# Kernel tuning notes

Measured on AMD Instinct MI355X. Metric: run time of the kernel, lower is better.

The kernel has to match this reference:

```python
import jax, jax.numpy as jnp
import numpy as np

N = 50000        # n_nodes
E = 800000       # n_edges (avg degree 16)
H = 64           # hidden_size
ALPHA = 0.5      # CRF alpha
BETA = 0.5       # CRF beta
N_LAYER = 2      # args.crf_layer
GAMMA = 0.2      # LeakyReLU negative slope


def setup_inputs() -> dict:
    key = jax.random.key(0)
    k = jax.random.split(key, 5)
    emb = jax.random.normal(k[0], (N, H), jnp.float32)
    W_fc = jax.random.normal(k[1], (H, H), jnp.float32) / np.sqrt(H)
    attn_fc_w = jax.random.normal(k[2], (1, 2 * H), jnp.float32) / np.sqrt(2 * H)
    src = jax.random.randint(k[3], (E,), 0, N, dtype=jnp.int32)
    dst = jax.random.randint(k[4], (E,), 0, N, dtype=jnp.int32)
    return {"emb": emb, "W_fc": W_fc, "attn_fc_w": attn_fc_w, "src": src, "dst": dst}


def _segment_softmax(e, dst, n):
    # softmax over incoming edges of each destination node (DGL mailbox softmax)
    m = jax.ops.segment_max(e, dst, num_segments=n)
    m = jnp.where(jnp.isfinite(m), m, 0.0)  # nodes with no in-edges
    ex = jnp.exp(e - m[dst])
    denom = jax.ops.segment_sum(ex, dst, num_segments=n)
    return ex / jnp.maximum(denom[dst], 1e-16)


def reference(emb, W_fc, attn_fc_w, src, dst):
    # attn_fc(concat(z_src, z_dst)) split into two per-node projections
    a_src = attn_fc_w[0, :H]
    a_dst = attn_fc_w[0, H:]
    h = emb
    e = None
    for _ in range(N_LAYER):
        z = h @ W_fc.T                              # [N, H] emb_attn
        e = (z @ a_src)[src] + (z @ a_dst)[dst]     # [E] edge logits
        e = jnp.where(e > 0, e, GAMMA * e)          # LeakyReLU(gamma)
        att = _segment_softmax(e, dst, N)           # [E]
        crf = jax.ops.segment_sum(att[:, None] * h[src], dst, num_segments=N)  # [N, H]
        h = (ALPHA * emb + BETA * crf) / (ALPHA + BETA)
    # training loss (is_train=True); reuses last layer's edge logits e
    loss_a = jnp.sum((h - emb) ** 2, axis=-1)                     # [N]
    att = _segment_softmax(e, dst, N)
    diff = jnp.sqrt(jnp.sum((h[dst] - h[src]) ** 2, axis=-1) + 1e-12)  # [E] L2 norm
    loss_b = jax.ops.segment_sum(att * diff, dst, num_segments=N)  # [N]
    loss = jnp.mean(ALPHA * loss_a + BETA * loss_b)
    return h, loss
```

## Files before the change

### kernel.cpp

```cpp
#include <hip/hip_runtime.h>

#define NNODES 50000
#define NEDGES 800000
#define HDIM 64
#define CAP 64
#define GAMMA 0.2f
#define SCAN_B 256
#define SCAN_NB ((NNODES + SCAN_B - 1) / SCAN_B)
#define LOSS_GRID 2048
#define NPART 8
#define NODES_PER_PART ((NNODES + NPART - 1) / NPART)
#define FILL_SLICES 192
#define E4 (NEDGES / 4)
#define CHUNK ((E4 + FILL_SLICES - 1) / FILL_SLICES)

typedef unsigned short u16;
typedef unsigned int u32;

__device__ __forceinline__ u16 f2bf(float f) {
    u32 u = __float_as_uint(f);
    u32 r = (u + 0x7FFFu + ((u >> 16) & 1u)) >> 16;
    return (u16)r;
}
__device__ __forceinline__ float bflo(u32 u) { return __uint_as_float(u << 16); }
__device__ __forceinline__ float bfhi(u32 u) { return __uint_as_float(u & 0xFFFF0000u); }

__device__ __forceinline__ float wave_sum(float v) {
    #pragma unroll
    for (int off = 32; off; off >>= 1) v += __shfl_xor(v, off, 64);
    return v;
}
__device__ __forceinline__ float wave_max(float v) {
    #pragma unroll
    for (int off = 32; off; off >>= 1) v = fmaxf(v, __shfl_xor(v, off, 64));
    return v;
}
__device__ __forceinline__ int wave_sum_i(int v) {
    #pragma unroll
    for (int off = 32; off; off >>= 1) v += __shfl_xor(v, off, 64);
    return v;
}
__device__ __forceinline__ float group8_sum(float v) {
    v += __shfl_xor(v, 1, 64);
    v += __shfl_xor(v, 2, 64);
    v += __shfl_xor(v, 4, 64);
    return v;
}

__global__ __launch_bounds__(256) void k_init(int* __restrict__ cursor,
                                              float* __restrict__ lossAcc,
                                              const float* __restrict__ Wfc,
                                              const float* __restrict__ attn,
                                              float* __restrict__ ws, float* __restrict__ wd) {
    int t = threadIdx.x;
    int idx = blockIdx.x * 256 + t;
    if (idx < NNODES) cursor[idx] = 0;
    if (blockIdx.x == gridDim.x - 1) {
        if (t >= 80 && t < 96) lossAcc[t - 80] = 0.f;
        if (t >= 128) {
            int tt = t - 128;
            int k = tt & 63;
            const float* av = attn + ((tt >= 64) ? HDIM : 0);
            float s = 0.f;
            for (int j = 0; j < HDIM; ++j) s += Wfc[j * HDIM + k] * av[j];
            if (tt < 64) ws[k] = s; else wd[k] = s;
        }
    }
}

__global__ __launch_bounds__(256) void k_fillx(const int4* __restrict__ src4,
                                               const int4* __restrict__ dst4,
                                               int* __restrict__ cursor,
                                               u16* __restrict__ padded) {
    const int part = blockIdx.x & (NPART - 1);
    const int slice = blockIdx.x >> 3;
    const int lo = slice * CHUNK;
    const int hi = min(lo + CHUNK, E4);
    const int plo = part * NODES_PER_PART;
    const int phi = plo + NODES_PER_PART;
    for (int i = lo + threadIdx.x; i < hi; i += 256) {
        int4 d = dst4[i];
        bool mx = d.x >= plo && d.x < phi;
        bool my = d.y >= plo && d.y < phi;
        bool mz = d.z >= plo && d.z < phi;
        bool mw = d.w >= plo && d.w < phi;
        if (mx | my | mz | mw) {
            int4 s = src4[i];
            if (mx) { int p0 = atomicAdd(&cursor[d.x], 1); if (p0 < CAP) padded[d.x * CAP + p0] = (u16)s.x; }
            if (my) { int p1 = atomicAdd(&cursor[d.y], 1); if (p1 < CAP) padded[d.y * CAP + p1] = (u16)s.y; }
            if (mz) { int p2 = atomicAdd(&cursor[d.z], 1); if (p2 < CAP) padded[d.z * CAP + p2] = (u16)s.z; }
            if (mw) { int p3 = atomicAdd(&cursor[d.w], 1); if (p3 < CAP) padded[d.w * CAP + p3] = (u16)s.w; }
        }
    }
}

__global__ __launch_bounds__(256) void k_scan1z(const int* __restrict__ deg,
                                                int* __restrict__ blockSums,
                                                const float* __restrict__ emb,
                                                const float* __restrict__ ws,
                                                const float* __restrict__ wd,
                                                u16* __restrict__ emb_bf,
                                                float* __restrict__ zs, float* __restrict__ zd) {
    int t = threadIdx.x;
    if (blockIdx.x < SCAN_NB) {
        int idx = blockIdx.x * SCAN_B + t;
        int v = (idx < NNODES) ? min(deg[idx], CAP) : 0;
        int wsum = wave_sum_i(v);
        __shared__ int part[4];
        if ((t & 63) == 0) part[t >> 6] = wsum;
        __syncthreads();
        if (t == 0) blockSums[blockIdx.x] = part[0] + part[1] + part[2] + part[3];
    }
    int tid = blockIdx.x * blockDim.x + threadIdx.x;
    int wid = tid >> 6;
    int lane = tid & 63;
    if (wid < NNODES) {
        float v = emb[wid * HDIM + lane];
        emb_bf[wid * HDIM + lane] = f2bf(v);
        float a = wave_sum(v * ws[lane]);
        float b = wave_sum(v * wd[lane]);
        if (lane == 0) { zs[wid] = a; zd[wid] = b; }
    }
}

__global__ __launch_bounds__(SCAN_B) void k_scan3(const int* __restrict__ deg,
                                                  const int* __restrict__ blockSums,
                                                  int* __restrict__ row_ptr) {
    __shared__ int s[SCAN_B];
    int t = threadIdx.x;
    int bv = (t < SCAN_NB) ? blockSums[t] : 0;
    s[t] = bv;
    __syncthreads();
    for (int off = 1; off < SCAN_B; off <<= 1) {
        int x = (t >= off) ? s[t - off] : 0;
        __syncthreads();
        s[t] += x;
        __syncthreads();
    }
    int blockOff = (blockIdx.x > 0) ? s[blockIdx.x - 1] : 0;
    __syncthreads();
    int idx = blockIdx.x * SCAN_B + t;
    int v = (idx < NNODES) ? min(deg[idx], CAP) : 0;
    s[t] = v;
    __syncthreads();
    for (int off = 1; off < SCAN_B; off <<= 1) {
        int x = (t >= off) ? s[t - off] : 0;
        __syncthreads();
        s[t] += x;
        __syncthreads();
    }
    if (idx < NNODES) {
        int excl = s[t] - v + blockOff;
        row_ptr[idx] = excl;
        if (idx == NNODES - 1) row_ptr[NNODES] = excl + v;
    }
}

template <bool STORE_ATT, bool COMPUTE_Z, bool WRITE_F32, bool STORE_LA, bool COMPACT>
__global__ __launch_bounds__(256) void k_layer(const u16* __restrict__ hbf_in,
                                               const float* __restrict__ emb,
                                               const int* __restrict__ deg,
                                               const int* __restrict__ row_ptr,
                                               const u16* __restrict__ padded,
                                               const float* __restrict__ zs,
                                               const float* __restrict__ zd,
                                               float* __restrict__ att_csr,
                                               u16* __restrict__ csr_c,
                                               u16* __restrict__ dmap_c,
                                               float* __restrict__ h_out,
                                               u16* __restrict__ hbf_out,
                                               const float* __restrict__ ws,
                                               const float* __restrict__ wd,
                                               float* __restrict__ zs_out,
                                               float* __restrict__ zd_out,
                                               float* __restrict__ la) {
    int wid = (blockIdx.x * blockDim.x + threadIdx.x) >> 6;
    int lane = threadIdx.x & 63;
    if (wid >= NNODES) return;
    int ne = min(deg[wid], CAP);
    int s0 = 0;
    if (STORE_ATT || COMPACT) s0 = row_ptr[wid];
    float zdn = zd[wid];
    const int sub8 = lane >> 3, q8 = lane & 7;
    float acc[8];
    #pragma unroll
    for (int i = 0; i < 8; ++i) acc[i] = 0.f;

    int s = 0; float e = -INFINITY;
    bool valid = lane < ne;
    if (valid) {
        s = padded[(size_t)wid * CAP + lane];
        float z = zs[s] + zdn;
        e = z > 0.f ? z : GAMMA * z;
    }
    float m = wave_max(e);
    float ex = valid ? __expf(e - m) : 0.f;
    float dsum = wave_sum(ex);
    float inv = 1.f / fmaxf(dsum, 1e-16f);
    if (STORE_ATT && valid) att_csr[s0 + lane] = ex * inv;
    if (COMPACT && valid) {
        csr_c[s0 + lane] = (u16)s;
        dmap_c[s0 + lane] = (u16)wid;
    }
    for (int j = 0; j < ne; j += 16) {
        int ja = j + sub8, jb = j + 8 + sub8;
        float wa = __shfl(ex, ja, 64);
        float wb = __shfl(ex, jb, 64);
        int ta = __shfl(s, ja, 64);
        int tb = __shfl(s, jb, 64);
        const uint4 ra = *(const uint4*)&hbf_in[(size_t)ta * HDIM + 8 * q8];
        const uint4 rb = *(const uint4*)&hbf_in[(size_t)tb * HDIM + 8 * q8];
        acc[0] += wa * bflo(ra.x) + wb * bflo(rb.x);
        acc[1] += wa * bfhi(ra.x) + wb * bfhi(rb.x);
        acc[2] += wa * bflo(ra.y) + wb * bflo(rb.y);
        acc[3] += wa * bfhi(ra.y) + wb * bfhi(rb.y);
        acc[4] += wa * bflo(ra.z) + wb * bflo(rb.z);
        acc[5] += wa * bfhi(ra.z) + wb * bfhi(rb.z);
        acc[6] += wa * bflo(ra.w) + wb * bflo(rb.w);
        acc[7] += wa * bfhi(ra.w) + wb * bfhi(rb.w);
    }
    #pragma unroll
    for (int off = 8; off <= 32; off <<= 1) {
        #pragma unroll
        for (int i = 0; i < 8; ++i) acc[i] += __shfl_xor(acc[i], off, 64);
    }
    float hv[8];
    #pragma unroll
    for (int i = 0; i < 8; ++i) hv[i] = 0.f;
    float lap = 0.f;
    if (sub8 == 0) {
        const float4 e0 = *(const float4*)&emb[(size_t)wid * HDIM + 8 * q8];
        const float4 e1 = *(const float4*)&emb[(size_t)wid * HDIM + 8 * q8 + 4];
        hv[0] = 0.5f * (e0.x + acc[0] * inv);
        hv[1] = 0.5f * (e0.y + acc[1] * inv);
        hv[2] = 0.5f * (e0.z + acc[2] * inv);
        hv[3] = 0.5f * (e0.w + acc[3] * inv);
        hv[4] = 0.5f * (e1.x + acc[4] * inv);
        hv[5] = 0.5f * (e1.y + acc[5] * inv);
        hv[6] = 0.5f * (e1.z + acc[6] * inv);
        hv[7] = 0.5f * (e1.w + acc[7] * inv);
        if (WRITE_F32) {
            *(float4*)&h_out[(size_t)wid * HDIM + 8 * q8]     = make_float4(hv[0], hv[1], hv[2], hv[3]);
            *(float4*)&h_out[(size_t)wid * HDIM + 8 * q8 + 4] = make_float4(hv[4], hv[5], hv[6], hv[7]);
        }
        uint4 o;
        o.x = (u32)f2bf(hv[0]) | ((u32)f2bf(hv[1]) << 16);
        o.y = (u32)f2bf(hv[2]) | ((u32)f2bf(hv[3]) << 16);
        o.z = (u32)f2bf(hv[4]) | ((u32)f2bf(hv[5]) << 16);
        o.w = (u32)f2bf(hv[6]) | ((u32)f2bf(hv[7]) << 16);
        *(uint4*)&hbf_out[(size_t)wid * HDIM + 8 * q8] = o;
        if (STORE_LA) {
            float d0 = hv[0] - e0.x, d1 = hv[1] - e0.y, d2 = hv[2] - e0.z, d3 = hv[3] - e0.w;
            float d4 = hv[4] - e1.x, d5 = hv[5] - e1.y, d6 = hv[6] - e1.z, d7 = hv[7] - e1.w;
            lap = d0 * d0 + d1 * d1 + d2 * d2 + d3 * d3 +
                  d4 * d4 + d5 * d5 + d6 * d6 + d7 * d7;
        }
    }
    if (STORE_LA) {
        float lsum = wave_sum(lap);
        if (lane == 0) la[wid] = lsum;
    }
    if (COMPUTE_Z) {
        float pa = 0.f, pb = 0.f;
        if (sub8 == 0) {
            const float4 w0 = *(const float4*)&ws[8 * q8];
            const float4 w1 = *(const float4*)&ws[8 * q8 + 4];
            const float4 d0 = *(const float4*)&wd[8 * q8];
            const float4 d1 = *(const float4*)&wd[8 * q8 + 4];
            pa = hv[0] * w0.x + hv[1] * w0.y + hv[2] * w0.z + hv[3] * w0.w +
                 hv[4] * w1.x + hv[5] * w1.y + hv[6] * w1.z + hv[7] * w1.w;
            pb = hv[0] * d0.x + hv[1] * d0.y + hv[2] * d0.z + hv[3] * d0.w +
                 hv[4] * d1.x + hv[5] * d1.y + hv[6] * d1.z + hv[7] * d1.w;
        }
        float a = wave_sum(pa);
        float b = wave_sum(pb);
        if (lane == 0) { zs_out[wid] = a; zd_out[wid] = b; }
    }
}

__global__ __launch_bounds__(256) void k_loss(const float* __restrict__ la,
                                              const u16* __restrict__ hbf,
                                              const u16* __restrict__ csr_src,
                                              const u16* __restrict__ dst_map,
                                              const float* __restrict__ att_csr,
                                              float* __restrict__ acc) {
    const int lane = threadIdx.x & 63;
    const int wib = threadIdx.x >> 6;
    const int gtid = blockIdx.x * blockDim.x + threadIdx.x;
    const int nthreads = gridDim.x * blockDim.x;
    const int gw = gtid >> 6;
    const int nwaves = nthreads >> 6;
    const int sub8 = lane >> 3, q8 = lane & 7;
    float lb = 0.f;

    for (int i = gtid; i < NNODES / 4; i += nthreads) {
        const float4 v = *(const float4*)&la[i * 4];
        lb += 0.5f * (v.x + v.y + v.z + v.w);
    }
    if ((NNODES & 3) != 0 && gtid < (NNODES & 3)) lb += 0.5f * la[(NNODES & ~3) + gtid];

    for (int g = gw; g < NEDGES / 32; g += nwaves) {
        int e0 = g * 32 + sub8;
        int e1 = e0 + 8, e2 = e0 + 16, e3 = e0 + 24;
        int s0i = csr_src[e0], d0i = dst_map[e0];
        int s1i = csr_src[e1], d1i = dst_map[e1];
        int s2i = csr_src[e2], d2i = dst_map[e2];
        int s3i = csr_src[e3], d3i = dst_map[e3];
        const uint4 rs0 = *(const uint4*)&hbf[(size_t)s0i * HDIM + 8 * q8];
        const uint4 rd0 = *(const uint4*)&hbf[(size_t)d0i * HDIM + 8 * q8];
        const uint4 rs1 = *(const uint4*)&hbf[(size_t)s1i * HDIM + 8 * q8];
        const uint4 rd1 = *(const uint4*)&hbf[(size_t)d1i * HDIM + 8 * q8];
        const uint4 rs2 = *(const uint4*)&hbf[(size_t)s2i * HDIM + 8 * q8];
        const uint4 rd2 = *(const uint4*)&hbf[(size_t)d2i * HDIM + 8 * q8];
        const uint4 rs3 = *(const uint4*)&hbf[(size_t)s3i * HDIM + 8 * q8];
        const uint4 rd3 = *(const uint4*)&hbf[(size_t)d3i * HDIM + 8 * q8];
        float a0 = bflo(rd0.x) - bflo(rs0.x), a1 = bfhi(rd0.x) - bfhi(rs0.x);
        float a2 = bflo(rd0.y) - bflo(rs0.y), a3 = bfhi(rd0.y) - bfhi(rs0.y);
        float a4 = bflo(rd0.z) - bflo(rs0.z), a5 = bfhi(rd0.z) - bfhi(rs0.z);
        float a6 = bflo(rd0.w) - bflo(rs0.w), a7 = bfhi(rd0.w) - bfhi(rs0.w);
        float b0 = bflo(rd1.x) - bflo(rs1.x), b1 = bfhi(rd1.x) - bfhi(rs1.x);
        float b2 = bflo(rd1.y) - bflo(rs1.y), b3 = bfhi(rd1.y) - bfhi(rs1.y);
        float b4 = bflo(rd1.z) - bflo(rs1.z), b5 = bfhi(rd1.z) - bfhi(rs1.z);
        float b6 = bflo(rd1.w) - bflo(rs1.w), b7 = bfhi(rd1.w) - bfhi(rs1.w);
        float c0 = bflo(rd2.x) - bflo(rs2.x), c1 = bfhi(rd2.x) - bfhi(rs2.x);
        float c2 = bflo(rd2.y) - bflo(rs2.y), c3 = bfhi(rd2.y) - bfhi(rs2.y);
        float c4 = bflo(rd2.z) - bflo(rs2.z), c5 = bfhi(rd2.z) - bfhi(rs2.z);
        float c6 = bflo(rd2.w) - bflo(rs2.w), c7 = bfhi(rd2.w) - bfhi(rs2.w);
        float g0 = bflo(rd3.x) - bflo(rs3.x), g1 = bfhi(rd3.x) - bfhi(rs3.x);
        float g2 = bflo(rd3.y) - bflo(rs3.y), g3 = bfhi(rd3.y) - bfhi(rs3.y);
        float g4 = bflo(rd3.z) - bflo(rs3.z), g5 = bfhi(rd3.z) - bfhi(rs3.z);
        float g6 = bflo(rd3.w) - bflo(rs3.w), g7 = bfhi(rd3.w) - bfhi(rs3.w);
        float ss0 = group8_sum(a0 * a0 + a1 * a1 + a2 * a2 + a3 * a3 +
                               a4 * a4 + a5 * a5 + a6 * a6 + a7 * a7);
        float ss1 = group8_sum(b0 * b0 + b1 * b1 + b2 * b2 + b3 * b3 +
                               b4 * b4 + b5 * b5 + b6 * b6 + b7 * b7);
        float ss2 = group8_sum(c0 * c0 + c1 * c1 + c2 * c2 + c3 * c3 +
                               c4 * c4 + c5 * c5 + c6 * c6 + c7 * c7);
        float ss3 = group8_sum(g0 * g0 + g1 * g1 + g2 * g2 + g3 * g3 +
                               g4 * g4 + g5 * g5 + g6 * g6 + g7 * g7);
        if (q8 == 0)
            lb += 0.5f * (att_csr[e0] * sqrtf(ss0 + 1e-12f) +
                          att_csr[e1] * sqrtf(ss1 + 1e-12f) +
                          att_csr[e2] * sqrtf(ss2 + 1e-12f) +
                          att_csr[e3] * sqrtf(ss3 + 1e-12f));
    }
    lb = wave_sum(lb);
    __shared__ float part[4];
    if (lane == 0) part[wib] = lb;
    __syncthreads();
    if (threadIdx.x == 0)
        atomicAdd(acc, part[0] + part[1] + part[2] + part[3]);
}

__global__ void k_finalize(const float* __restrict__ acc, float* __restrict__ out_loss) {
    out_loss[0] = acc[0] / (float)NNODES;
}

extern "C" void kernel_launch(void* const* d_in, const int* in_sizes, int n_in,
                              void* d_out, int out_size, void* d_ws, size_t ws_size,
                              hipStream_t stream) {
    const float* emb  = (const float*)d_in[0];
    const float* Wfc  = (const float*)d_in[1];
    const float* attn = (const float*)d_in[2];
    const int*   src  = (const int*)d_in[3];
    const int*   dst  = (const int*)d_in[4];
    float* out = (float*)d_out;

    char* p = (char*)d_ws;
    int*   cursor  = (int*)p;   p += (size_t)NNODES * 4;
    float* lossAcc = (float*)p; p += 256;
    int*   row_ptr = (int*)p;   p += (size_t)(NNODES + 1) * 4;
    int*   bsums   = (int*)p;   p += (size_t)SCAN_NB * 4;
    float* wsv     = (float*)p; p += 64 * 4;
    float* wdv     = (float*)p; p += 64 * 4;
    float* zs0     = (float*)p; p += (size_t)NNODES * 4;
    float* zd0     = (float*)p; p += (size_t)NNODES * 4;
    float* zs1     = (float*)p; p += (size_t)NNODES * 4;
    float* zd1     = (float*)p; p += (size_t)NNODES * 4;
    float* laArr   = (float*)p; p += (size_t)NNODES * 4;
    float* att_csr = (float*)p; p += (size_t)NEDGES * 4;
    p = (char*)(((size_t)p + 255) & ~(size_t)255);
    u16*   padded  = (u16*)p;   p += (size_t)NNODES * CAP * 2;
    u16*   csr_src = (u16*)p;   p += (size_t)NEDGES * 2;
    u16*   dst_map = (u16*)p;   p += (size_t)NEDGES * 2;
    u16*   emb_bf  = (u16*)p;   p += (size_t)NNODES * HDIM * 2;
    u16*   h1_bf   = (u16*)p;   p += (size_t)NNODES * HDIM * 2;
    u16*   out_bf  = (u16*)p;   p += (size_t)NNODES * HDIM * 2;

    const int NB = (NNODES + 3) / 4;

    k_init<<<SCAN_NB, 256, 0, stream>>>(cursor, lossAcc, Wfc, attn, wsv, wdv);
    k_fillx<<<NPART * FILL_SLICES, 256, 0, stream>>>((const int4*)src, (const int4*)dst,
                                                     cursor, padded);
    k_scan1z<<<NB, 256, 0, stream>>>(cursor, bsums, emb, wsv, wdv, emb_bf, zs0, zd0);
    k_scan3<<<SCAN_NB, SCAN_B, 0, stream>>>(cursor, bsums, row_ptr);

    k_layer<false, true, false, false, true><<<NB, 256, 0, stream>>>(
        emb_bf, emb, cursor, row_ptr, padded, zs0, zd0,
        att_csr, csr_src, dst_map, out , h1_bf, wsv, wdv, zs1, zd1, laArr);
    k_layer<true, false, true, true, false><<<NB, 256, 0, stream>>>(
        h1_bf, emb, cursor, row_ptr, padded, zs1, zd1,
        att_csr, csr_src, dst_map, out, out_bf, wsv, wdv, zs0, zd0, laArr);

    k_loss<<<LOSS_GRID, 256, 0, stream>>>(laArr, out_bf, csr_src, dst_map, att_csr, lossAcc);
    k_finalize<<<1, 1, 0, stream>>>(lossAcc, out + (size_t)NNODES * HDIM);
}
```

Measured before the change: 228.3 us.

## Replace prefix-scan row pointers with atomic per-block edge offset allocation

Removes the two-pass degree scan (blockSums reduction and a separate scan kernel) and instead has each block of the first layer kernel reserve a contiguous edge range via one atomicAdd on a global counter, storing per-node base offsets for the second layer. This saves a kernel launch and the scan's work and syncs. In exchange the compacted edge order becomes nondeterministic across blocks, and the early-return bounds check was dropped, relying on NNODES being a multiple of 4. edgeCnt must be zeroed elsewhere, presumably in k_init.

```diff
diff --git a/kernel.cpp b/kernel.cpp
--- a/kernel.cpp
+++ b/kernel.cpp
@@ -5,8 +5,7 @@
 #define HDIM 64
 #define CAP 64
 #define GAMMA 0.2f
-#define SCAN_B 256
-#define SCAN_NB ((NNODES + SCAN_B - 1) / SCAN_B)
+#define SCAN_NB ((NNODES + 255) / 256)
 #define LOSS_GRID 2048
 #define NPART 8
 #define NODES_PER_PART ((NNODES + NPART - 1) / NPART)
@@ -33,11 +32,6 @@
 __device__ __forceinline__ float wave_max(float v) {
     #pragma unroll
     for (int off = 32; off; off >>= 1) v = fmaxf(v, __shfl_xor(v, off, 64));
-    return v;
-}
-__device__ __forceinline__ int wave_sum_i(int v) {
-    #pragma unroll
-    for (int off = 32; off; off >>= 1) v += __shfl_xor(v, off, 64);
     return v;
 }
 __device__ __forceinline__ float group8_sum(float v) {
@@ -94,73 +88,28 @@
     }
 }
 
-__global__ __launch_bounds__(256) void k_scan1z(const int* __restrict__ deg,
-                                                int* __restrict__ blockSums,
-                                                const float* __restrict__ emb,
-                                                const float* __restrict__ ws,
-                                                const float* __restrict__ wd,
-                                                u16* __restrict__ emb_bf,
-                                                float* __restrict__ zs, float* __restrict__ zd) {
-    int t = threadIdx.x;
-    if (blockIdx.x < SCAN_NB) {
-        int idx = blockIdx.x * SCAN_B + t;
-        int v = (idx < NNODES) ? min(deg[idx], CAP) : 0;
-        int wsum = wave_sum_i(v);
-        __shared__ int part[4];
-        if ((t & 63) == 0) part[t >> 6] = wsum;
-        __syncthreads();
-        if (t == 0) blockSums[blockIdx.x] = part[0] + part[1] + part[2] + part[3];
-    }
+__global__ __launch_bounds__(256) void k_zinit(const float* __restrict__ emb,
+                                               const float* __restrict__ ws,
+                                               const float* __restrict__ wd,
+                                               u16* __restrict__ emb_bf,
+                                               float* __restrict__ zs, float* __restrict__ zd) {
     int tid = blockIdx.x * blockDim.x + threadIdx.x;
     int wid = tid >> 6;
     int lane = tid & 63;
-    if (wid < NNODES) {
-        float v = emb[wid * HDIM + lane];
-        emb_bf[wid * HDIM + lane] = f2bf(v);
-        float a = wave_sum(v * ws[lane]);
-        float b = wave_sum(v * wd[lane]);
-        if (lane == 0) { zs[wid] = a; zd[wid] = b; }
-    }
-}
-
-__global__ __launch_bounds__(SCAN_B) void k_scan3(const int* __restrict__ deg,
-                                                  const int* __restrict__ blockSums,
-                                                  int* __restrict__ row_ptr) {
-    __shared__ int s[SCAN_B];
-    int t = threadIdx.x;
-    int bv = (t < SCAN_NB) ? blockSums[t] : 0;
-    s[t] = bv;
-    __syncthreads();
-    for (int off = 1; off < SCAN_B; off <<= 1) {
-        int x = (t >= off) ? s[t - off] : 0;
-        __syncthreads();
-        s[t] += x;
-        __syncthreads();
-    }
-    int blockOff = (blockIdx.x > 0) ? s[blockIdx.x - 1] : 0;
-    __syncthreads();
-    int idx = blockIdx.x * SCAN_B + t;
-    int v = (idx < NNODES) ? min(deg[idx], CAP) : 0;
-    s[t] = v;
-    __syncthreads();
-    for (int off = 1; off < SCAN_B; off <<= 1) {
-        int x = (t >= off) ? s[t - off] : 0;
-        __syncthreads();
-        s[t] += x;
-        __syncthreads();
-    }
-    if (idx < NNODES) {
-        int excl = s[t] - v + blockOff;
-        row_ptr[idx] = excl;
-        if (idx == NNODES - 1) row_ptr[NNODES] = excl + v;
-    }
+    if (wid >= NNODES) return;
+    float v = emb[wid * HDIM + lane];
+    emb_bf[wid * HDIM + lane] = f2bf(v);
+    float a = wave_sum(v * ws[lane]);
+    float b = wave_sum(v * wd[lane]);
+    if (lane == 0) { zs[wid] = a; zd[wid] = b; }
 }
 
 template <bool STORE_ATT, bool COMPUTE_Z, bool WRITE_F32, bool STORE_LA, bool COMPACT>
 __global__ __launch_bounds__(256) void k_layer(const u16* __restrict__ hbf_in,
                                                const float* __restrict__ emb,
                                                const int* __restrict__ deg,
-                                               const int* __restrict__ row_ptr,
+                                               int* __restrict__ base,
+                                               int* __restrict__ edgeCnt,
                                                const u16* __restrict__ padded,
                                                const float* __restrict__ zs,
                                                const float* __restrict__ zd,
@@ -176,10 +125,24 @@
                                                float* __restrict__ la) {
     int wid = (blockIdx.x * blockDim.x + threadIdx.x) >> 6;
     int lane = threadIdx.x & 63;
-    if (wid >= NNODES) return;
+    int wib = threadIdx.x >> 6;
     int ne = min(deg[wid], CAP);
     int s0 = 0;
-    if (STORE_ATT || COMPACT) s0 = row_ptr[wid];
+    __shared__ int wb[4];
+    if (COMPACT) {
+        if (lane == 0) wb[wib] = ne;
+        __syncthreads();
+        if (threadIdx.x == 0) {
+            int t0 = wb[0], t1 = wb[1], t2 = wb[2], t3 = wb[3];
+            int b = atomicAdd(edgeCnt, t0 + t1 + t2 + t3);
+            wb[0] = b; wb[1] = b + t0; wb[2] = b + t0 + t1; wb[3] = b + t0 + t1 + t2;
+        }
+        __syncthreads();
+        s0 = wb[wib];
+        if (lane == 0) base[wid] = s0;
+    } else if (STORE_ATT) {
+        s0 = base[wid];
+    }
     float zdn = zd[wid];
     const int sub8 = lane >> 3, q8 = lane & 7;
     float acc[8];
@@ -205,19 +168,19 @@
     for (int j = 0; j < ne; j += 16) {
         int ja = j + sub8, jb = j + 8 + sub8;
         float wa = __shfl(ex, ja, 64);
-        float wb = __shfl(ex, jb, 64);
+        float wbv = __shfl(ex, jb, 64);
         int ta = __shfl(s, ja, 64);
         int tb = __shfl(s, jb, 64);
         const uint4 ra = *(const uint4*)&hbf_in[(size_t)ta * HDIM + 8 * q8];
         const uint4 rb = *(const uint4*)&hbf_in[(size_t)tb * HDIM + 8 * q8];
-        acc[0] += wa * bflo(ra.x) + wb * bflo(rb.x);
-        acc[1] += wa * bfhi(ra.x) + wb * bfhi(rb.x);
-        acc[2] += wa * bflo(ra.y) + wb * bflo(rb.y);
-        acc[3] += wa * bfhi(ra.y) + wb * bfhi(rb.y);
-        acc[4] += wa * bflo(ra.z) + wb * bflo(rb.z);
-        acc[5] += wa * bfhi(ra.z) + wb * bfhi(rb.z);
-        acc[6] += wa * bflo(ra.w) + wb * bflo(rb.w);
-        acc[7] += wa * bfhi(ra.w) + wb * bfhi(rb.w);
+        acc[0] += wa * bflo(ra.x) + wbv * bflo(rb.x);
+        acc[1] += wa * bfhi(ra.x) + wbv * bfhi(rb.x);
+        acc[2] += wa * bflo(ra.y) + wbv * bflo(rb.y);
+        acc[3] += wa * bfhi(ra.y) + wbv * bfhi(rb.y);
+        acc[4] += wa * bflo(ra.z) + wbv * bflo(rb.z);
+        acc[5] += wa * bfhi(ra.z) + wbv * bfhi(rb.z);
+        acc[6] += wa * bflo(ra.w) + wbv * bflo(rb.w);
+        acc[7] += wa * bfhi(ra.w) + wbv * bfhi(rb.w);
     }
     #pragma unroll
     for (int off = 8; off <= 32; off <<= 1) {
@@ -368,9 +331,10 @@
 
     char* p = (char*)d_ws;
     int*   cursor  = (int*)p;   p += (size_t)NNODES * 4;
-    float* lossAcc = (float*)p; p += 256;
-    int*   row_ptr = (int*)p;   p += (size_t)(NNODES + 1) * 4;
-    int*   bsums   = (int*)p;   p += (size_t)SCAN_NB * 4;
+    float* lossAcc = (float*)p;
+    int*   edgeCnt = (int*)(p + 4);
+    p += 256;
+    int*   baseArr = (int*)p;   p += (size_t)NNODES * 4;
     float* wsv     = (float*)p; p += 64 * 4;
     float* wdv     = (float*)p; p += 64 * 4;
     float* zs0     = (float*)p; p += (size_t)NNODES * 4;
@@ -392,14 +356,13 @@
     k_init<<<SCAN_NB, 256, 0, stream>>>(cursor, lossAcc, Wfc, attn, wsv, wdv);
     k_fillx<<<NPART * FILL_SLICES, 256, 0, stream>>>((const int4*)src, (const int4*)dst,
                                                      cursor, padded);
-    k_scan1z<<<NB, 256, 0, stream>>>(cursor, bsums, emb, wsv, wdv, emb_bf, zs0, zd0);
-    k_scan3<<<SCAN_NB, SCAN_B, 0, stream>>>(cursor, bsums, row_ptr);
+    k_zinit<<<NB, 256, 0, stream>>>(emb, wsv, wdv, emb_bf, zs0, zd0);
 
     k_layer<false, true, false, false, true><<<NB, 256, 0, stream>>>(
-        emb_bf, emb, cursor, row_ptr, padded, zs0, zd0,
+        emb_bf, emb, cursor, baseArr, edgeCnt, padded, zs0, zd0,
         att_csr, csr_src, dst_map, out , h1_bf, wsv, wdv, zs1, zd1, laArr);
     k_layer<true, false, true, true, false><<<NB, 256, 0, stream>>>(
-        h1_bf, emb, cursor, row_ptr, padded, zs1, zd1,
+        h1_bf, emb, cursor, baseArr, edgeCnt, padded, zs1, zd1,
         att_csr, csr_src, dst_map, out, out_bf, wsv, wdv, zs0, zd0, laArr);
 
     k_loss<<<LOSS_GRID, 256, 0, stream>>>(laArr, out_bf, csr_src, dst_map, att_csr, lossAcc);
```

After: 343.5 us. 50.4% more time.
